# Performance work log

Measured on AMD Instinct MI355X. Metric: run time of the kernel, lower is better.

Reference implementation:

```python
import jax, jax.numpy as jnp
import numpy as np

B, S, D = 8, 2048, 2048          # batch, seq, hidden
E, K, NSTEPS = 16, 2, 4          # routed experts, top_k, routers
NSH = 2                          # shared experts
DR = D // 4                      # routed inner dim (routed_ratio=4)
DS = D // 2                      # shared inner dim (shared_ratio=2)


def setup_inputs() -> dict:
    key = jax.random.key(0)
    ks = jax.random.split(key, 8)
    s = 0.02
    return {
        "x": jax.random.normal(ks[0], (B, S, D), jnp.float32),
        "step_t": 1,
        "router_w": jax.random.normal(ks[1], (NSTEPS, D, E), jnp.float32) * s,
        "re_w1": jax.random.normal(ks[2], (E, D, DR), jnp.float32) * s,
        "re_b1": jnp.zeros((E, DR), jnp.float32),
        "re_w2": jax.random.normal(ks[3], (E, DR, D), jnp.float32) * s,
        "re_b2": jnp.zeros((E, D), jnp.float32),
        "sh_w1": jax.random.normal(ks[4], (NSH, D, DS), jnp.float32) * s,
        "sh_b1": jnp.zeros((NSH, DS), jnp.float32),
        "sh_w2": jax.random.normal(ks[5], (NSH, DS, D), jnp.float32) * s,
        "sh_b2": jnp.zeros((NSH, D), jnp.float32),
    }


def reference(x, step_t, router_w, re_w1, re_b1, re_w2, re_b2, sh_w1, sh_b1, sh_w2, sh_b2):
    orig = x.shape
    flat = x.reshape(-1, orig[-1])                       # [T, D]
    T = flat.shape[0]

    # shared expert group: sum of always-active experts
    h = jax.nn.silu(jnp.einsum('td,sdk->tsk', flat, sh_w1) + sh_b1)   # [T, NSH, DS]
    out = jnp.einsum('tsk,skd->td', h, sh_w2) + sh_b2.sum(0)          # [T, D]

    # top-k router for this step (eval mode: no jitter noise)
    logits = flat @ router_w[step_t]                     # [T, E]
    probs = jax.nn.softmax(logits, axis=-1)
    w, idx = jax.lax.top_k(probs, K)                     # [T, K]

    # combine weights per (token, expert): sum_k w_k * 1[idx_k == e]
    cw = jnp.zeros((T, E), flat.dtype).at[jnp.arange(T)[:, None], idx].add(w)

    # routed experts: masked gather-compute-scatter expressed as
    # weighted accumulation (zero combine-weight == token not routed)
    def body(acc, p):
        w1, b1, w2, b2, cwe = p                          # cwe: [T]
        ye = jax.nn.silu(flat @ w1 + b1) @ w2 + b2       # [T, D]
        return acc + cwe[:, None] * ye, None

    out, _ = jax.lax.scan(body, out, (re_w1, re_b1, re_w2, re_b2, cw.T))
    return out.reshape(orig)
```

## Files before the change

kernel.cpp:

```cpp
#include <hip/hip_runtime.h>
#include <hip/hip_bf16.h>
#include <stdint.h>


#define DEV static __device__ __forceinline__

typedef __attribute__((ext_vector_type(8))) short bf16x8;
typedef __attribute__((ext_vector_type(4))) float f32x4;

constexpr int T_TOK = 16384;
constexpr int DIM   = 2048;
constexpr int NEXP  = 16;
constexpr int DR_K  = 512;
constexpr int DS_K  = 1024;
constexpr int MAXROWS = 34816;
constexpr int MAXTILES = 272;

DEV void gload16(const void* g, void* l) {
  __builtin_amdgcn_global_load_lds(
      (const __attribute__((address_space(1))) unsigned int*)g,
      (__attribute__((address_space(3))) unsigned int*)l, 16, 0, 0);
}

DEV float silu_f(float v) { return v / (1.f + __expf(-v)); }

__global__ __launch_bounds__(256) void cast_router_kernel(
    const float* __restrict__ x, __hip_bfloat16* __restrict__ xb,
    const float* __restrict__ rw_all, const int* __restrict__ step_p,
    int* __restrict__ tk_idx, float* __restrict__ tk_w) {
  int tid = threadIdx.x;
  int t0 = blockIdx.x * 8;
  __shared__ float xs[8][1024];
  __shared__ float red[4][4][8][4];

  float acc[8][4];
#pragma unroll
  for (int tk = 0; tk < 8; ++tk)
#pragma unroll
    for (int j = 0; j < 4; ++j) acc[tk][j] = 0.f;

  const float* rwbase = rw_all + (size_t)step_p[0] * DIM * NEXP;

#pragma unroll
  for (int half = 0; half < 2; ++half) {
#pragma unroll
    for (int tk = 0; tk < 8; ++tk) {
      const float4* xp = (const float4*)(x + (size_t)(t0 + tk) * DIM + half * 1024);
      float4 v = xp[tid];
      *(float4*)&xs[tk][tid * 4] = v;
      union { ushort4 u; __hip_bfloat16 h[4]; } o;
      o.h[0] = __float2bfloat16(v.x); o.h[1] = __float2bfloat16(v.y);
      o.h[2] = __float2bfloat16(v.z); o.h[3] = __float2bfloat16(v.w);
      *(ushort4*)(xb + (size_t)(t0 + tk) * DIM + half * 1024 + tid * 4) = o.u;
    }
    __syncthreads();
    const float4* rw4 = (const float4*)(rwbase + (size_t)half * 1024 * NEXP);
#pragma unroll 4
    for (int i = 0; i < 16; ++i) {
      int c = i * 256 + tid;
      int d = c >> 2;
      float4 wv = rw4[c];
#pragma unroll
      for (int tk = 0; tk < 8; ++tk) {
        float v = xs[tk][d];
        acc[tk][0] += v * wv.x; acc[tk][1] += v * wv.y;
        acc[tk][2] += v * wv.z; acc[tk][3] += v * wv.w;
      }
    }
    __syncthreads();
  }

#pragma unroll
  for (int m = 4; m < 64; m <<= 1) {
#pragma unroll
    for (int tk = 0; tk < 8; ++tk) {
      acc[tk][0] += __shfl_xor(acc[tk][0], m);
      acc[tk][1] += __shfl_xor(acc[tk][1], m);
      acc[tk][2] += __shfl_xor(acc[tk][2], m);
      acc[tk][3] += __shfl_xor(acc[tk][3], m);
    }
  }
  int lane = tid & 63, wvi = tid >> 6;
  if (lane < 4) {
#pragma unroll
    for (int tk = 0; tk < 8; ++tk) {
      float4 r = {acc[tk][0], acc[tk][1], acc[tk][2], acc[tk][3]};
      *(float4*)&red[wvi][lane][tk][0] = r;
    }
  }
  __syncthreads();
  if (tid < 8) {
    int t = t0 + tid;
    float lg[16];
#pragma unroll
    for (int e = 0; e < 16; ++e) {
      int cg = e >> 2, j = e & 3;
      lg[e] = red[0][cg][tid][j] + red[1][cg][tid][j] +
              red[2][cg][tid][j] + red[3][cg][tid][j];
    }
    float mx = lg[0];
    for (int i = 1; i < 16; ++i) mx = fmaxf(mx, lg[i]);
    float pr[16], sum = 0.f;
    for (int i = 0; i < 16; ++i) { pr[i] = expf(lg[i] - mx); sum += pr[i]; }
    float inv = 1.f / sum;
    int b0 = -1, b1 = -1; float w0 = -1.f, w1 = -1.f;
    for (int i = 0; i < 16; ++i) {
      float v = pr[i] * inv;
      if (v > w0)      { w1 = w0; b1 = b0; w0 = v; b0 = i; }
      else if (v > w1) { w1 = v; b1 = i; }
    }
    tk_idx[2 * t] = b0; tk_idx[2 * t + 1] = b1;
    tk_w[2 * t] = w0;   tk_w[2 * t + 1] = w1;
  }
}

__global__ __launch_bounds__(256) void hist_kernel(const int* __restrict__ tk_idx,
                                                   int* __restrict__ cnt_pad) {
  __shared__ int lc[16];
  int tid = threadIdx.x;
  if (tid < 16) lc[tid] = 0;
  __syncthreads();
  int base = blockIdx.x * 2048;
#pragma unroll
  for (int i = 0; i < 8; ++i)
    atomicAdd(&lc[tk_idx[base + i * 256 + tid]], 1);
  __syncthreads();
  if (tid < 16) atomicAdd(&cnt_pad[tid * 16], lc[tid]);
}

__global__ __launch_bounds__(256) void transpose_cast(const float* __restrict__ in,
                                                      __hip_bfloat16* __restrict__ out,
                                                      int R, int C) {
  __shared__ float t[64][68];
  size_t bo = (size_t)blockIdx.z * R * C;
  in += bo; out += bo;
  int c0 = blockIdx.x * 64, r0 = blockIdx.y * 64;
  int tid = threadIdx.x;
  int rr = tid >> 2, cc0 = (tid & 3) * 16;
  const float* ip = in + (size_t)(r0 + rr) * C + c0 + cc0;
#pragma unroll
  for (int j = 0; j < 4; ++j)
    *(float4*)&t[rr][cc0 + 4 * j] = *(const float4*)(ip + 4 * j);
  __syncthreads();
  int wr = tid >> 2, wc0 = (tid & 3) * 16;
  union { bf16x8 v; __hip_bfloat16 h[8]; } o0, o1;
#pragma unroll
  for (int k = 0; k < 8; ++k) o0.h[k] = __float2bfloat16(t[wc0 + k][wr]);
#pragma unroll
  for (int k = 0; k < 8; ++k) o1.h[k] = __float2bfloat16(t[wc0 + 8 + k][wr]);
  __hip_bfloat16* op = out + (size_t)(c0 + wr) * R + r0 + wc0;
  *(bf16x8*)op = o0.v;
  *(bf16x8*)(op + 8) = o1.v;
}

__global__ void scan_kernel(const int* __restrict__ cnt_pad, int* __restrict__ seg,
                            int* __restrict__ padded, int* __restrict__ tile_e,
                            int* __restrict__ tile_m0, int* __restrict__ n_tiles) {
  if (threadIdx.x == 0) {
    int off = 0, nt = 0;
    for (int e = 0; e < NEXP; ++e) {
      seg[e] = off;
      int pc = (cnt_pad[e * 16] + 127) & ~127;
      padded[e] = pc;
      for (int m = 0; m < pc; m += 128) { tile_e[nt] = e; tile_m0[nt] = m; ++nt; }
      off += pc;
    }
    seg[NEXP] = off;
    n_tiles[0] = nt;
  }
}

__global__ __launch_bounds__(256) void scatter_kernel(
    const int* __restrict__ tk_idx, const float* __restrict__ tk_w,
    const int* __restrict__ seg, int* __restrict__ cnt2_pad,
    int* __restrict__ tok_list, float* __restrict__ w_list,
    int* __restrict__ pos_list) {
  __shared__ int lh[16], lbase[16];
  int tid = threadIdx.x;
  if (tid < 16) lh[tid] = 0;
  __syncthreads();
  int t = blockIdx.x * 256 + tid;
  int e0 = tk_idx[2 * t], e1 = tk_idx[2 * t + 1];
  int s0 = atomicAdd(&lh[e0], 1);
  int s1 = atomicAdd(&lh[e1], 1);
  __syncthreads();
  if (tid < 16) lbase[tid] = atomicAdd(&cnt2_pad[tid * 16], lh[tid]);
  __syncthreads();
  int p0 = seg[e0] + lbase[e0] + s0;
  int p1 = seg[e1] + lbase[e1] + s1;
  tok_list[p0] = t; w_list[p0] = tk_w[2 * t];     pos_list[2 * t] = p0;
  tok_list[p1] = t; w_list[p1] = tk_w[2 * t + 1]; pos_list[2 * t + 1] = p1;
}

__global__ void pad_kernel(const int* __restrict__ cnt_pad, const int* __restrict__ padded,
                           const int* __restrict__ seg, int* __restrict__ tok_list,
                           float* __restrict__ w_list) {
  int e = blockIdx.x;
  int c = cnt_pad[e * 16], pc = padded[e], s = seg[e];
  for (int i = c + threadIdx.x; i < pc; i += blockDim.x) {
    tok_list[s + i] = 0;
    w_list[s + i] = 0.f;
  }
}

DEV void swz_tile(int bid, int NB, int& tile, int& nb) {
  tile = 8 * (bid / (8 * NB)) + (bid & 7);
  nb = (bid >> 3) % NB;
}

template <int MODE>
DEV void gemm_shared(const __hip_bfloat16* __restrict__ Abase,
                     const __hip_bfloat16* __restrict__ Bt,
                     const float* __restrict__ bias,
                     __hip_bfloat16* __restrict__ outb,
                     float* __restrict__ outf) {
  constexpr int KD = DIM;
  constexpr int NT = KD / 32;

  int tid = threadIdx.x;
  int ln = tid & 63, w8 = tid >> 6;
  int wm = w8 >> 2, wn = w8 & 3;
  int tile, nb;
  swz_tile(blockIdx.x, 8, tile, nb);
  int m0 = tile * 256;
  int n0 = nb * 256;

  __shared__ __align__(16) char lds[2 * 32768];

  int srow = tid >> 2;
  int schunk = (tid & 3) ^ ((tid >> 3) & 3);
  const __hip_bfloat16 *aS0, *aS1, *bS0, *bS1;
  {
    int ar0 = m0 + srow, ar1 = m0 + 128 + srow;
    int br0, br1;
    if constexpr (MODE == 0) {
      int s = n0 >> 10, nn = n0 & 1023;
      br0 = s * DS_K + nn + srow; br1 = s * DS_K + nn + 128 + srow;
    } else { br0 = n0 + srow; br1 = n0 + 128 + srow; }
    aS0 = Abase + (size_t)ar0 * KD + schunk * 8;
    aS1 = Abase + (size_t)ar1 * KD + schunk * 8;
    bS0 = Bt + (size_t)br0 * KD + schunk * 8;
    bS1 = Bt + (size_t)br1 * KD + schunk * 8;
  }
  int wlds = w8 * 1024;

  {
    gload16(aS0, lds + wlds);
    gload16(aS1, lds + 8192 + wlds);
    gload16(bS0, lds + 16384 + wlds);
    gload16(bS1, lds + 16384 + 8192 + wlds);
  }
  asm volatile("s_waitcnt vmcnt(0)" ::: "memory");
  __builtin_amdgcn_s_barrier();

  f32x4 acc[8][4];
#pragma unroll
  for (int i = 0; i < 8; ++i)
#pragma unroll
    for (int j = 0; j < 4; ++j) acc[i][j] = (f32x4){0.f, 0.f, 0.f, 0.f};

  int rof = (ln & 15) * 64 + ((((ln >> 4) ^ (ln >> 1)) & 3) << 4);
  int aoffs = wm * 8192 + rof;
  int boffs = 16384 + wn * 4096 + rof;

#pragma unroll 2
  for (int t = 0; t < NT; ++t) {
    const char* sl = lds + (t & 1) * 32768;
    char* dst = lds + ((t + 1) & 1) * 32768;
    bool pf = (t + 1) < NT;
    int ko = (t + 1) * 32;
    bf16x8 af[4], bfr[4];

    if (pf) {
      gload16(aS0 + ko, dst + wlds);
      gload16(aS1 + ko, dst + 8192 + wlds);
    }
#pragma unroll
    for (int fi = 0; fi < 4; ++fi)
      af[fi] = *(const bf16x8*)(sl + aoffs + fi * 1024);
#pragma unroll
    for (int ni = 0; ni < 4; ++ni)
      bfr[ni] = *(const bf16x8*)(sl + boffs + ni * 1024);
    __builtin_amdgcn_s_barrier();
    __builtin_amdgcn_s_setprio(1);
#pragma unroll
    for (int fi = 0; fi < 4; ++fi)
#pragma unroll
      for (int ni = 0; ni < 4; ++ni)
        acc[fi][ni] = __builtin_amdgcn_mfma_f32_16x16x32_bf16(af[fi], bfr[ni], acc[fi][ni], 0, 0, 0);
    __builtin_amdgcn_s_setprio(0);
    __builtin_amdgcn_s_barrier();

    if (pf) {
      gload16(bS0 + ko, dst + 16384 + wlds);
      gload16(bS1 + ko, dst + 16384 + 8192 + wlds);
    }
#pragma unroll
    for (int fi = 0; fi < 4; ++fi)
      af[fi] = *(const bf16x8*)(sl + aoffs + 4096 + fi * 1024);
    __builtin_amdgcn_s_barrier();
    __builtin_amdgcn_s_setprio(1);
#pragma unroll
    for (int fi = 0; fi < 4; ++fi)
#pragma unroll
      for (int ni = 0; ni < 4; ++ni)
        acc[4 + fi][ni] = __builtin_amdgcn_mfma_f32_16x16x32_bf16(af[fi], bfr[ni], acc[4 + fi][ni], 0, 0, 0);
    __builtin_amdgcn_s_setprio(0);

    if (pf) {
      asm volatile("s_waitcnt vmcnt(0)" ::: "memory");
      __builtin_amdgcn_s_barrier();
    }
  }

  int colc = ln & 15;
  int rowb = (ln >> 4) << 2;
#pragma unroll
  for (int mi = 0; mi < 8; ++mi) {
    int mlb = wm * 128 + mi * 16 + rowb;
#pragma unroll
    for (int ni = 0; ni < 4; ++ni) {
      int ng = n0 + wn * 64 + ni * 16 + colc;
#pragma unroll
      for (int j = 0; j < 4; ++j) {
        float v = acc[mi][ni][j];
        int ml = mlb + j;
        if constexpr (MODE == 0) {
          float s = silu_f(v + bias[ng]);
          outb[(size_t)(m0 + ml) * 2048 + ng] = __float2bfloat16(s);
        } else {
          outf[(size_t)(m0 + ml) * DIM + ng] = v + bias[ng] + bias[DIM + ng];
        }
      }
    }
  }
}

template <int MODE, int NB>
DEV void gemm_routed(const __hip_bfloat16* __restrict__ Abase,
                     const __hip_bfloat16* __restrict__ Bt,
                     const float* __restrict__ bias,
                     __hip_bfloat16* __restrict__ outb,
                     const int* __restrict__ tok_list,
                     const float* __restrict__ w_list,
                     const int* __restrict__ seg_off,
                     const int* __restrict__ tile_e,
                     const int* __restrict__ tile_m0,
                     const int* __restrict__ n_tiles) {
  constexpr int KD = (MODE == 3) ? DR_K : DIM;
  constexpr int NT = KD / 32;

  int tid = threadIdx.x;
  int ln = tid & 63, w8 = tid >> 6;
  int wm = w8 >> 2, wn = w8 & 3;

  __shared__ __align__(16) char lds[3 * 24576];
  __shared__ int tk_s[128];
  __shared__ float w_s[128];

  int W = n_tiles[0] * NB;
  int q = (W + 7) >> 3;
  int xcd = blockIdx.x & 7, k = blockIdx.x >> 3;
  if (k >= q) return;
  int w = xcd * q + k;
  if (w >= W) return;
  int tl = w / NB, nb = w % NB;

  int e = tile_e[tl];
  int m0 = tile_m0[tl];
  int n0 = nb * 256;
  int seg = seg_off[e];
  if (tid < 128) {
    if constexpr (MODE == 2) tk_s[tid] = tok_list[seg + m0 + tid];
    w_s[tid] = w_list[seg + m0 + tid];
  }
  __syncthreads();

  int srow = tid >> 2;
  int schunk = (tid & 3) ^ ((tid >> 3) & 3);
  const __hip_bfloat16 *aS, *bS0, *bS1;
  {
    int ar, br0;
    if constexpr (MODE == 2) { ar = tk_s[srow]; br0 = e * DR_K + n0 + srow; }
    else                     { ar = seg + m0 + srow; br0 = e * DIM + n0 + srow; }
    aS  = Abase + (size_t)ar * KD + schunk * 8;
    bS0 = Bt + (size_t)br0 * KD + schunk * 8;
    bS1 = bS0 + (size_t)128 * KD;
  }
  int wlds = w8 * 1024;

#pragma unroll
  for (int tt = 0; tt < 2; ++tt) {
    char* sl = lds + tt * 24576;
    int ko = tt * 32;
    gload16(aS + ko, sl + wlds);
    gload16(bS0 + ko, sl + 8192 + wlds);
    gload16(bS1 + ko, sl + 16384 + wlds);
  }
  asm volatile("s_waitcnt vmcnt(3)" ::: "memory");
  __builtin_amdgcn_s_barrier();

  f32x4 acc[4][4];
#pragma unroll
  for (int i = 0; i < 4; ++i)
#pragma unroll
    for (int j = 0; j < 4; ++j) acc[i][j] = (f32x4){0.f, 0.f, 0.f, 0.f};

  int rof = (ln & 15) * 64 + ((((ln >> 4) ^ (ln >> 1)) & 3) << 4);
  int aoffs = wm * 4096 + rof;
  int boffs = 8192 + wn * 4096 + rof;

  int s0 = 0;
  for (int t = 0; t < NT; ++t) {
    const char* sl = lds + s0 * 24576;
    int sd = s0 - 1; if (sd < 0) sd += 3;
    char* dst = lds + sd * 24576;
    bool pf = (t + 2) < NT;
    int ko = (t + 2) * 32;

    if (pf) {
      gload16(aS + ko, dst + wlds);
      gload16(bS0 + ko, dst + 8192 + wlds);
      gload16(bS1 + ko, dst + 16384 + wlds);
    }
    bf16x8 af[4], bfr[4];
#pragma unroll
    for (int fi = 0; fi < 4; ++fi)
      af[fi] = *(const bf16x8*)(sl + aoffs + fi * 1024);
#pragma unroll
    for (int ni = 0; ni < 4; ++ni)
      bfr[ni] = *(const bf16x8*)(sl + boffs + ni * 1024);
    __builtin_amdgcn_s_barrier();
    __builtin_amdgcn_s_setprio(1);
#pragma unroll
    for (int fi = 0; fi < 4; ++fi)
#pragma unroll
      for (int ni = 0; ni < 4; ++ni)
        acc[fi][ni] = __builtin_amdgcn_mfma_f32_16x16x32_bf16(af[fi], bfr[ni], acc[fi][ni], 0, 0, 0);
    __builtin_amdgcn_s_setprio(0);

    if (t + 1 < NT) {
      if (pf) asm volatile("s_waitcnt vmcnt(3)" ::: "memory");
      else    asm volatile("s_waitcnt vmcnt(0)" ::: "memory");
      __builtin_amdgcn_s_barrier();
    }
    s0 = (s0 + 1 == 3) ? 0 : s0 + 1;
  }

  int colc = ln & 15;
  int rowb = (ln >> 4) << 2;
#pragma unroll
  for (int mi = 0; mi < 4; ++mi) {
    int mlb = wm * 64 + mi * 16 + rowb;
#pragma unroll
    for (int ni = 0; ni < 4; ++ni) {
      int ng = n0 + wn * 64 + ni * 16 + colc;
#pragma unroll
      for (int j = 0; j < 4; ++j) {
        float v = acc[mi][ni][j];
        int ml = mlb + j;
        if constexpr (MODE == 2) {
          float s = silu_f(v + bias[(size_t)e * DR_K + ng]) * w_s[ml];
          outb[((size_t)seg + m0 + ml) * DR_K + ng] = __float2bfloat16(s);
        } else {
          float wv = w_s[ml];
          outb[((size_t)seg + m0 + ml) * DIM + ng] =
              __float2bfloat16(v + wv * bias[(size_t)e * DIM + ng]);
        }
      }
    }
  }
}

__global__ __launch_bounds__(512) void gemm_sh_l1(
    const __hip_bfloat16* A, const __hip_bfloat16* B, const float* bias,
    __hip_bfloat16* ob, float* of) {
  gemm_shared<0>(A, B, bias, ob, of);
}
__global__ __launch_bounds__(512) void gemm_sh_l2(
    const __hip_bfloat16* A, const __hip_bfloat16* B, const float* bias,
    __hip_bfloat16* ob, float* of) {
  gemm_shared<1>(A, B, bias, ob, of);
}
__global__ __launch_bounds__(512) void gemm_re_l1(
    const __hip_bfloat16* A, const __hip_bfloat16* B, const float* bias,
    __hip_bfloat16* ob, const int* tok, const float* wl, const int* seg,
    const int* tl_e, const int* tl_m0, const int* ntl) {
  gemm_routed<2, 2>(A, B, bias, ob, tok, wl, seg, tl_e, tl_m0, ntl);
}
__global__ __launch_bounds__(512) void gemm_re_l2(
    const __hip_bfloat16* A, const __hip_bfloat16* B, const float* bias,
    __hip_bfloat16* ob, const int* tok, const float* wl, const int* seg,
    const int* tl_e, const int* tl_m0, const int* ntl) {
  gemm_routed<3, 8>(A, B, bias, ob, tok, wl, seg, tl_e, tl_m0, ntl);
}

__global__ __launch_bounds__(256) void combine_kernel(float* __restrict__ out,
                                                      const __hip_bfloat16* __restrict__ y_re,
                                                      const int* __restrict__ pos_list) {
  int t = blockIdx.x;
  int d0 = threadIdx.x << 3;
  int p0 = pos_list[2 * t], p1 = pos_list[2 * t + 1];
  union { bf16x8 v; __hip_bfloat16 h[8]; } a, b;
  a.v = *(const bf16x8*)(y_re + (size_t)p0 * DIM + d0);
  b.v = *(const bf16x8*)(y_re + (size_t)p1 * DIM + d0);
  float* o = out + (size_t)t * DIM + d0;
  float4 o0 = *(float4*)o, o1 = *(float4*)(o + 4);
  o0.x += __bfloat162float(a.h[0]) + __bfloat162float(b.h[0]);
  o0.y += __bfloat162float(a.h[1]) + __bfloat162float(b.h[1]);
  o0.z += __bfloat162float(a.h[2]) + __bfloat162float(b.h[2]);
  o0.w += __bfloat162float(a.h[3]) + __bfloat162float(b.h[3]);
  o1.x += __bfloat162float(a.h[4]) + __bfloat162float(b.h[4]);
  o1.y += __bfloat162float(a.h[5]) + __bfloat162float(b.h[5]);
  o1.z += __bfloat162float(a.h[6]) + __bfloat162float(b.h[6]);
  o1.w += __bfloat162float(a.h[7]) + __bfloat162float(b.h[7]);
  *(float4*)o = o0;
  *(float4*)(o + 4) = o1;
}

extern "C" void kernel_launch(void* const* d_in, const int* in_sizes, int n_in,
                              void* d_out, int out_size, void* d_ws, size_t ws_size,
                              hipStream_t stream) {
  const float* x     = (const float*)d_in[0];
  const int* step_p  = (const int*)d_in[1];
  const float* rw    = (const float*)d_in[2];
  const float* re_w1 = (const float*)d_in[3];
  const float* re_b1 = (const float*)d_in[4];
  const float* re_w2 = (const float*)d_in[5];
  const float* re_b2 = (const float*)d_in[6];
  const float* sh_w1 = (const float*)d_in[7];
  const float* sh_b1 = (const float*)d_in[8];
  const float* sh_w2 = (const float*)d_in[9];
  const float* sh_b2 = (const float*)d_in[10];
  float* out = (float*)d_out;

  char* w = (char*)d_ws;
  auto take = [&](size_t bytes) {
    char* p = w;
    w += (bytes + 255) & ~(size_t)255;
    return p;
  };
  __hip_bfloat16* xb     = (__hip_bfloat16*)take((size_t)T_TOK * DIM * 2);
  __hip_bfloat16* h_sh   = (__hip_bfloat16*)take((size_t)T_TOK * 2048 * 2);
  __hip_bfloat16* w1t_sh = (__hip_bfloat16*)take((size_t)2 * DS_K * DIM * 2);
  __hip_bfloat16* w2t_sh = (__hip_bfloat16*)take((size_t)DIM * 2048 * 2);
  __hip_bfloat16* h_re   = (__hip_bfloat16*)take((size_t)MAXROWS * DR_K * 2);
  __hip_bfloat16* w1t_re = (__hip_bfloat16*)take((size_t)NEXP * DR_K * DIM * 2);
  __hip_bfloat16* w2t_re = (__hip_bfloat16*)take((size_t)NEXP * DIM * DR_K * 2);
  int* tk_idx   = (int*)take((size_t)T_TOK * 2 * 4);
  float* tk_w   = (float*)take((size_t)T_TOK * 2 * 4);
  int* ctrl     = (int*)take(4096);
  int* tok_list = (int*)take((size_t)MAXROWS * 4);
  float* w_list = (float*)take((size_t)MAXROWS * 4);
  int* pos_list = (int*)take((size_t)T_TOK * 2 * 4);
  int* tile_e   = (int*)take((size_t)MAXTILES * 4);
  int* tile_m0  = (int*)take((size_t)MAXTILES * 4);
  int* n_tiles  = (int*)take(256);
  int* cnt_pad  = ctrl;
  int* cnt2_pad = ctrl + 256;
  int* seg      = ctrl + 512;
  int* padded   = ctrl + 544;

  __hip_bfloat16* y_re = (__hip_bfloat16*)d_ws;

  hipMemsetAsync(ctrl, 0, 4096, stream);
  cast_router_kernel<<<T_TOK / 8, 256, 0, stream>>>(x, xb, rw, step_p, tk_idx, tk_w);
  transpose_cast<<<dim3(DS_K / 64, DIM / 64, 2), 256, 0, stream>>>(sh_w1, w1t_sh, DIM, DS_K);
  transpose_cast<<<dim3(DIM / 64, 2048 / 64, 1), 256, 0, stream>>>(sh_w2, w2t_sh, 2048, DIM);
  transpose_cast<<<dim3(DR_K / 64, DIM / 64, NEXP), 256, 0, stream>>>(re_w1, w1t_re, DIM, DR_K);
  transpose_cast<<<dim3(DIM / 64, DR_K / 64, NEXP), 256, 0, stream>>>(re_w2, w2t_re, DR_K, DIM);
  hist_kernel<<<16, 256, 0, stream>>>(tk_idx, cnt_pad);
  scan_kernel<<<1, 32, 0, stream>>>(cnt_pad, seg, padded, tile_e, tile_m0, n_tiles);
  scatter_kernel<<<T_TOK / 256, 256, 0, stream>>>(tk_idx, tk_w, seg, cnt2_pad,
                                                  tok_list, w_list, pos_list);
  pad_kernel<<<NEXP, 256, 0, stream>>>(cnt_pad, padded, seg, tok_list, w_list);

  gemm_sh_l1<<<64 * 8, 512, 0, stream>>>(xb, w1t_sh, sh_b1, h_sh, nullptr);
  gemm_re_l1<<<MAXTILES * 2, 512, 0, stream>>>(xb, w1t_re, re_b1, h_re,
                                               tok_list, w_list, seg,
                                               tile_e, tile_m0, n_tiles);
  gemm_sh_l2<<<64 * 8, 512, 0, stream>>>(h_sh, w2t_sh, sh_b2, nullptr, out);
  gemm_re_l2<<<MAXTILES * 8, 512, 0, stream>>>(h_re, w2t_re, re_b2, y_re,
                                               tok_list, w_list, seg,
                                               tile_e, tile_m0, n_tiles);
  combine_kernel<<<T_TOK, 256, 0, stream>>>(out, y_re, pos_list);
}
```

Before: 749.8 us.

## Deepen shared-expert GEMM K-tile to 64 with four-phase load/compute pipeline

The shared-expert GEMM now processes a 64-wide K slice per iteration instead of 32. This halves the number of main-loop iterations and the barriers that come with them. The LDS double buffer grows to 128 KB with a new XOR swizzle. Global prefetch is split into four phases interleaved with four MFMA quadrants. The larger LDS footprint can cut occupancy to one block per CU, and register pressure rises from the two-deep fragment arrays.

```diff
diff --git a/kernel.cpp b/kernel.cpp
--- a/kernel.cpp
+++ b/kernel.cpp
@@ -215,7 +215,7 @@
                      __hip_bfloat16* __restrict__ outb,
                      float* __restrict__ outf) {
   constexpr int KD = DIM;
-  constexpr int NT = KD / 32;
+  constexpr int NT = KD / 64;
 
   int tid = threadIdx.x;
   int ln = tid & 63, w8 = tid >> 6;
@@ -225,31 +225,36 @@
   int m0 = tile * 256;
   int n0 = nb * 256;
 
-  __shared__ __align__(16) char lds[2 * 32768];
-
-  int srow = tid >> 2;
-  int schunk = (tid & 3) ^ ((tid >> 3) & 3);
-  const __hip_bfloat16 *aS0, *aS1, *bS0, *bS1;
-  {
-    int ar0 = m0 + srow, ar1 = m0 + 128 + srow;
-    int br0, br1;
-    if constexpr (MODE == 0) {
-      int s = n0 >> 10, nn = n0 & 1023;
-      br0 = s * DS_K + nn + srow; br1 = s * DS_K + nn + 128 + srow;
-    } else { br0 = n0 + srow; br1 = n0 + 128 + srow; }
-    aS0 = Abase + (size_t)ar0 * KD + schunk * 8;
-    aS1 = Abase + (size_t)ar1 * KD + schunk * 8;
-    bS0 = Bt + (size_t)br0 * KD + schunk * 8;
-    bS1 = Bt + (size_t)br1 * KD + schunk * 8;
-  }
-  int wlds = w8 * 1024;
-
-  {
-    gload16(aS0, lds + wlds);
-    gload16(aS1, lds + 8192 + wlds);
-    gload16(bS0, lds + 16384 + wlds);
-    gload16(bS1, lds + 16384 + 8192 + wlds);
-  }
+  __shared__ __align__(16) char lds[2 * 65536];
+
+  int lrow = w8 * 8 + (ln >> 3);
+  int cg8 = (((ln & 7) ^ (ln >> 3)) << 3);
+  int browBase;
+  if constexpr (MODE == 0) {
+    int s = n0 >> 10, nn = n0 & 1023;
+    browBase = s * DS_K + nn;
+  } else {
+    browBase = n0;
+  }
+  const __hip_bfloat16 *aSrc[2][2], *bSrc[2][2];
+  int dA[2][2], dB[2][2];
+#pragma unroll
+  for (int h = 0; h < 2; ++h)
+#pragma unroll
+    for (int l = 0; l < 2; ++l) {
+      aSrc[h][l] = Abase + (size_t)(m0 + h * 128 + l * 64 + lrow) * KD + cg8;
+      bSrc[h][l] = Bt + (size_t)(browBase + h * 128 + l * 64 + lrow) * KD + cg8;
+      dA[h][l] = h * 16384 + (l * 8 + w8) * 1024;
+      dB[h][l] = 32768 + h * 16384 + (l * 8 + w8) * 1024;
+    }
+
+#pragma unroll
+  for (int h = 0; h < 2; ++h)
+#pragma unroll
+    for (int l = 0; l < 2; ++l) {
+      gload16(aSrc[h][l], lds + dA[h][l]);
+      gload16(bSrc[h][l], lds + dB[h][l]);
+    }
   asm volatile("s_waitcnt vmcnt(0)" ::: "memory");
   __builtin_amdgcn_s_barrier();
 
@@ -259,52 +264,104 @@
 #pragma unroll
     for (int j = 0; j < 4; ++j) acc[i][j] = (f32x4){0.f, 0.f, 0.f, 0.f};
 
-  int rof = (ln & 15) * 64 + ((((ln >> 4) ^ (ln >> 1)) & 3) << 4);
-  int aoffs = wm * 8192 + rof;
-  int boffs = 16384 + wn * 4096 + rof;
-
-#pragma unroll 2
+  int rbyte = (ln & 15) * 128;
+  int ch0 = (((ln >> 4) ^ (ln & 7)) << 4);
+  int ch1 = (((4 + (ln >> 4)) ^ (ln & 7)) << 4);
+  int aBase = wm * 16384 + rbyte;
+  int bBase = 32768 + wn * 8192 + rbyte;
+
+  bf16x8 af[4][2], bfr[4][2];
+
   for (int t = 0; t < NT; ++t) {
-    const char* sl = lds + (t & 1) * 32768;
-    char* dst = lds + ((t + 1) & 1) * 32768;
+    const char* buf = lds + (t & 1) * 65536;
+    char* nxt = lds + ((t + 1) & 1) * 65536;
     bool pf = (t + 1) < NT;
-    int ko = (t + 1) * 32;
-    bf16x8 af[4], bfr[4];
+    int ko = (t + 1) * 64;
 
     if (pf) {
-      gload16(aS0 + ko, dst + wlds);
-      gload16(aS1 + ko, dst + 8192 + wlds);
-    }
-#pragma unroll
-    for (int fi = 0; fi < 4; ++fi)
-      af[fi] = *(const bf16x8*)(sl + aoffs + fi * 1024);
-#pragma unroll
-    for (int ni = 0; ni < 4; ++ni)
-      bfr[ni] = *(const bf16x8*)(sl + boffs + ni * 1024);
+      gload16(aSrc[0][0] + ko, nxt + dA[0][0]);
+      gload16(aSrc[0][1] + ko, nxt + dA[0][1]);
+    }
+#pragma unroll
+    for (int mf = 0; mf < 4; ++mf) {
+      af[mf][0] = *(const bf16x8*)(buf + aBase + mf * 2048 + ch0);
+      af[mf][1] = *(const bf16x8*)(buf + aBase + mf * 2048 + ch1);
+    }
+#pragma unroll
+    for (int nf = 0; nf < 2; ++nf) {
+      bfr[nf][0] = *(const bf16x8*)(buf + bBase + nf * 2048 + ch0);
+      bfr[nf][1] = *(const bf16x8*)(buf + bBase + nf * 2048 + ch1);
+    }
     __builtin_amdgcn_s_barrier();
     __builtin_amdgcn_s_setprio(1);
 #pragma unroll
-    for (int fi = 0; fi < 4; ++fi)
-#pragma unroll
-      for (int ni = 0; ni < 4; ++ni)
-        acc[fi][ni] = __builtin_amdgcn_mfma_f32_16x16x32_bf16(af[fi], bfr[ni], acc[fi][ni], 0, 0, 0);
+    for (int mf = 0; mf < 4; ++mf)
+#pragma unroll
+      for (int nf = 0; nf < 2; ++nf)
+#pragma unroll
+        for (int kk = 0; kk < 2; ++kk)
+          acc[mf][nf] = __builtin_amdgcn_mfma_f32_16x16x32_bf16(
+              af[mf][kk], bfr[nf][kk], acc[mf][nf], 0, 0, 0);
     __builtin_amdgcn_s_setprio(0);
     __builtin_amdgcn_s_barrier();
 
     if (pf) {
-      gload16(bS0 + ko, dst + 16384 + wlds);
-      gload16(bS1 + ko, dst + 16384 + 8192 + wlds);
-    }
-#pragma unroll
-    for (int fi = 0; fi < 4; ++fi)
-      af[fi] = *(const bf16x8*)(sl + aoffs + 4096 + fi * 1024);
+      gload16(aSrc[1][0] + ko, nxt + dA[1][0]);
+      gload16(aSrc[1][1] + ko, nxt + dA[1][1]);
+    }
+#pragma unroll
+    for (int nf = 2; nf < 4; ++nf) {
+      bfr[nf][0] = *(const bf16x8*)(buf + bBase + nf * 2048 + ch0);
+      bfr[nf][1] = *(const bf16x8*)(buf + bBase + nf * 2048 + ch1);
+    }
     __builtin_amdgcn_s_barrier();
     __builtin_amdgcn_s_setprio(1);
 #pragma unroll
-    for (int fi = 0; fi < 4; ++fi)
-#pragma unroll
-      for (int ni = 0; ni < 4; ++ni)
-        acc[4 + fi][ni] = __builtin_amdgcn_mfma_f32_16x16x32_bf16(af[fi], bfr[ni], acc[4 + fi][ni], 0, 0, 0);
+    for (int mf = 0; mf < 4; ++mf)
+#pragma unroll
+      for (int nf = 2; nf < 4; ++nf)
+#pragma unroll
+        for (int kk = 0; kk < 2; ++kk)
+          acc[mf][nf] = __builtin_amdgcn_mfma_f32_16x16x32_bf16(
+              af[mf][kk], bfr[nf][kk], acc[mf][nf], 0, 0, 0);
+    __builtin_amdgcn_s_setprio(0);
+    __builtin_amdgcn_s_barrier();
+
+    if (pf) {
+      gload16(bSrc[0][0] + ko, nxt + dB[0][0]);
+      gload16(bSrc[0][1] + ko, nxt + dB[0][1]);
+    }
+#pragma unroll
+    for (int mf = 0; mf < 4; ++mf) {
+      af[mf][0] = *(const bf16x8*)(buf + aBase + (4 + mf) * 2048 + ch0);
+      af[mf][1] = *(const bf16x8*)(buf + aBase + (4 + mf) * 2048 + ch1);
+    }
+    __builtin_amdgcn_s_barrier();
+    __builtin_amdgcn_s_setprio(1);
+#pragma unroll
+    for (int mf = 0; mf < 4; ++mf)
+#pragma unroll
+      for (int nf = 0; nf < 2; ++nf)
+#pragma unroll
+        for (int kk = 0; kk < 2; ++kk)
+          acc[4 + mf][nf] = __builtin_amdgcn_mfma_f32_16x16x32_bf16(
+              af[mf][kk], bfr[nf][kk], acc[4 + mf][nf], 0, 0, 0);
+    __builtin_amdgcn_s_setprio(0);
+    __builtin_amdgcn_s_barrier();
+
+    if (pf) {
+      gload16(bSrc[1][0] + ko, nxt + dB[1][0]);
+      gload16(bSrc[1][1] + ko, nxt + dB[1][1]);
+    }
+    __builtin_amdgcn_s_setprio(1);
+#pragma unroll
+    for (int mf = 0; mf < 4; ++mf)
+#pragma unroll
+      for (int nf = 2; nf < 4; ++nf)
+#pragma unroll
+        for (int kk = 0; kk < 2; ++kk)
+          acc[4 + mf][nf] = __builtin_amdgcn_mfma_f32_16x16x32_bf16(
+              af[mf][kk], bfr[nf][kk], acc[4 + mf][nf], 0, 0, 0);
     __builtin_amdgcn_s_setprio(0);
 
     if (pf) {
```

Result: faster. 721.3 us (-3.8%).
